# Optimization experiments

Hardware: AMD Instinct MI355X
Metric: run time of the kernel (lower is better)

Reference implementation:

```python
import jax, jax.numpy as jnp
import numpy as np

N_RULE, N_TOKEN = 256, 32000
F_IN, F_ACT, H = 512, 512, 1024  # input_feature_size, action_feature_size, output_feature_size
L, B = 128, 64


def setup_inputs() -> dict:
    key = jax.random.key(0)
    ks = jax.random.split(key, 8)
    s_ih = 1.0 / np.sqrt(H)
    return {
        "input_feature": jax.random.normal(ks[0], (B, F_IN), dtype=jnp.float32),
        "previous_actions": jax.random.randint(ks[1], (L, B, 3), 0, N_RULE, dtype=jnp.int64),
        "mask": jnp.ones((L, B), dtype=jnp.float32),
        "hidden_state": jnp.zeros((B, H), dtype=jnp.float32),
        "state": jnp.zeros((B, H), dtype=jnp.float32),
        "rule_embed": jax.random.normal(ks[2], (N_RULE, F_ACT), dtype=jnp.float32),
        "token_embed": jax.random.normal(ks[3], (N_TOKEN, F_ACT), dtype=jnp.float32),
        "W_ih": jax.random.uniform(ks[4], (4 * H, F_IN + F_ACT), jnp.float32, -s_ih, s_ih),
        "W_hh": jax.random.uniform(ks[5], (4 * H, H), jnp.float32, -s_ih, s_ih),
        "b_ih": jax.random.uniform(ks[6], (4 * H,), jnp.float32, -s_ih, s_ih),
        "b_hh": jax.random.uniform(ks[7], (4 * H,), jnp.float32, -s_ih, s_ih),
    }


def _masked_embed(table, idx):
    # EmbeddingWithMask: index == -1 maps to the zero vector
    valid = (idx != -1)
    emb = table[jnp.where(valid, idx, 0)]
    return emb * valid[..., None].astype(table.dtype)


def reference(input_feature, previous_actions, mask, hidden_state, state,
              rule_embed, token_embed, W_ih, W_hh, b_ih, b_hh):
    prev_rules = previous_actions[..., 0]   # (L, B)
    prev_tokens = previous_actions[..., 1]  # (L, B)
    act = _masked_embed(rule_embed, prev_rules) + _masked_embed(token_embed, prev_tokens)  # (L,B,F_ACT)

    # Per-step input is concat([input_feature, act_t]); precompute the whole
    # input projection x @ W_ih^T + biases once (big batched GEMM).
    l, b = act.shape[0], act.shape[1]
    Wx, Wa = W_ih[:, :input_feature.shape[1]], W_ih[:, input_feature.shape[1]:]
    xg = (input_feature @ Wx.T)[None] + jnp.einsum('lba,ga->lbg', act, Wa) + (b_ih + b_hh)  # (L,B,4H)

    def step(carry, xg_t):
        h, c = carry
        g = xg_t + h @ W_hh.T                     # (B, 4H)
        i, f, gg, o = jnp.split(g, 4, axis=-1)    # torch LSTMCell gate order
        i, f, o = jax.nn.sigmoid(i), jax.nn.sigmoid(f), jax.nn.sigmoid(o)
        c1 = f * c + i * jnp.tanh(gg)
        h1 = o * jnp.tanh(c1)
        return (h1, c1), h1

    (h_n, c_n), hs = jax.lax.scan(step, (hidden_state, state), xg)
    return hs, h_n, c_n
```

## Files before the change

### kernel.cpp

```cpp
#include <hip/hip_runtime.h>
#include <hip/hip_bf16.h>

typedef __attribute__((ext_vector_type(8))) short bf16x8;
typedef __attribute__((ext_vector_type(4))) float f32x4;

#define L_SEQ 128
#define BATCH 64
#define HID   1024
#define GATES 4096
#define NWG   256
#define UPW   4
#define FSTR  32

__device__ inline short f2bf_s(float f) {
  __hip_bfloat16 h = __float2bfloat16(f);
  union { __hip_bfloat16 hh; short s; } u; u.hh = h; return u.s;
}
__device__ inline float sigm(float x) { return 1.f / (1.f + __expf(-x)); }
__device__ inline float tanh_f(float x) {
  x = fminf(x, 15.f);
  float e = __expf(2.f * x);
  return (e - 1.f) / (e + 1.f);
}

__global__ void k_init(const float* __restrict__ hidden, const float* __restrict__ x,
                       const float* __restrict__ bih, const float* __restrict__ bhh,
                       __hip_bfloat16* __restrict__ h_all0, __hip_bfloat16* __restrict__ x_bf,
                       float* __restrict__ bias2, unsigned* __restrict__ bar) {
  int gid = blockIdx.x * 256 + threadIdx.x;
  if (gid < BATCH * HID) h_all0[gid] = __float2bfloat16(hidden[gid]);
  if (gid < BATCH * 512) x_bf[gid]  = __float2bfloat16(x[gid]);
  if (gid < GATES)       bias2[gid] = bih[gid] + bhh[gid];
  if (gid < 16384)       bar[gid] = 0u;
}

__global__ void k_wsplit(const float* __restrict__ Wih,
                         __hip_bfloat16* __restrict__ Wx, __hip_bfloat16* __restrict__ Wa) {
  int e = blockIdx.x * 256 + threadIdx.x;
  int g = e >> 7;
  int ko = (e & 127) << 3;
  const float* src = Wih + (size_t)g * 1024 + ko;
  float4 f0 = *(const float4*)(src);
  float4 f1 = *(const float4*)(src + 4);
  union { bf16x8 v; short s[8]; } o;
  o.s[0]=f2bf_s(f0.x); o.s[1]=f2bf_s(f0.y); o.s[2]=f2bf_s(f0.z); o.s[3]=f2bf_s(f0.w);
  o.s[4]=f2bf_s(f1.x); o.s[5]=f2bf_s(f1.y); o.s[6]=f2bf_s(f1.z); o.s[7]=f2bf_s(f1.w);
  if (ko < 512) *(bf16x8*)(Wx + (size_t)g * 512 + ko)        = o.v;
  else          *(bf16x8*)(Wa + (size_t)g * 512 + (ko - 512)) = o.v;
}

__global__ void k_act(const int* __restrict__ pa, const float* __restrict__ remb,
                      const float* __restrict__ temb, __hip_bfloat16* __restrict__ act) {
  int row = blockIdx.x;
  int tid = threadIdx.x;
  int r  = pa[row * 3 + 0];
  int tk = pa[row * 3 + 1];
  float sr = (r  != -1) ? 1.f : 0.f; int ri = (r  != -1) ? r  : 0;
  float st = (tk != -1) ? 1.f : 0.f; int ti = (tk != -1) ? tk : 0;
  const float4* rr = (const float4*)(remb + (size_t)ri * 512);
  const float4* tr = (const float4*)(temb + (size_t)ti * 512);
  float4 a = rr[tid * 2], b4 = rr[tid * 2 + 1];
  float4 c4 = tr[tid * 2], d4 = tr[tid * 2 + 1];
  union { bf16x8 v; short s[8]; } o;
  o.s[0]=f2bf_s(sr*a.x + st*c4.x);  o.s[1]=f2bf_s(sr*a.y + st*c4.y);
  o.s[2]=f2bf_s(sr*a.z + st*c4.z);  o.s[3]=f2bf_s(sr*a.w + st*c4.w);
  o.s[4]=f2bf_s(sr*b4.x + st*d4.x); o.s[5]=f2bf_s(sr*b4.y + st*d4.y);
  o.s[6]=f2bf_s(sr*b4.z + st*d4.z); o.s[7]=f2bf_s(sr*b4.w + st*d4.w);
  *(bf16x8*)(act + (size_t)row * 512 + tid * 8) = o.v;
}

template<int MODE>
__global__ __launch_bounds__(256) void k_gemm(
    const __hip_bfloat16* __restrict__ A, const __hip_bfloat16* __restrict__ B,
    const float* __restrict__ addend, float* __restrict__ Cf,
    __hip_bfloat16* __restrict__ Cb, int M) {
  __shared__ __hip_bfloat16 At[128][72];
  __shared__ __hip_bfloat16 Bt[128][72];
  const int tid = threadIdx.x;
  const int m0 = blockIdx.y * 128, n0 = blockIdx.x * 128;
  const int w = tid >> 6, lane = tid & 63;
  const int wm = (w >> 1) * 64, wn = (w & 1) * 64;
  const int lm = lane & 15, quad = lane >> 4;
  const int srow = tid >> 1, shalf = (tid & 1) * 32;
  f32x4 acc[4][4] = {};
  for (int k0 = 0; k0 < 512; k0 += 64) {
    int arow = m0 + srow;
    if (MODE == 0 && arow >= M) arow = M - 1;
    const bf16x8* ag = (const bf16x8*)(A + (size_t)arow * 512 + k0 + shalf);
    const bf16x8* bg = (const bf16x8*)(B + (size_t)(n0 + srow) * 512 + k0 + shalf);
    bf16x8 av[4], bv[4];
#pragma unroll
    for (int q = 0; q < 4; ++q) { av[q] = ag[q]; bv[q] = bg[q]; }
    __syncthreads();
#pragma unroll
    for (int q = 0; q < 4; ++q) {
      *(bf16x8*)(&At[srow][shalf + q * 8]) = av[q];
      *(bf16x8*)(&Bt[srow][shalf + q * 8]) = bv[q];
    }
    __syncthreads();
#pragma unroll
    for (int ks = 0; ks < 2; ++ks) {
      bf16x8 af[4], bf[4];
#pragma unroll
      for (int i = 0; i < 4; ++i) {
        af[i] = *(const bf16x8*)(&At[wm + i * 16 + lm][ks * 32 + quad * 8]);
        bf[i] = *(const bf16x8*)(&Bt[wn + i * 16 + lm][ks * 32 + quad * 8]);
      }
#pragma unroll
      for (int i = 0; i < 4; ++i)
#pragma unroll
        for (int j = 0; j < 4; ++j)
          acc[i][j] = __builtin_amdgcn_mfma_f32_16x16x32_bf16(af[i], bf[j], acc[i][j], 0, 0, 0);
    }
  }
#pragma unroll
  for (int i = 0; i < 4; ++i) {
    int mrow = m0 + wm + i * 16 + quad * 4;
#pragma unroll
    for (int j = 0; j < 4; ++j) {
      int ncol = n0 + wn + j * 16 + lm;
#pragma unroll
      for (int r = 0; r < 4; ++r) {
        int m = mrow + r;
        if (MODE == 0) {
          if (m < M) Cf[(size_t)m * GATES + ncol] = acc[i][j][r] + addend[ncol];
        } else {
          float v = acc[i][j][r] + addend[(size_t)(m & 63) * GATES + ncol];
          Cb[(size_t)m * GATES + ncol] = __float2bfloat16(v);
        }
      }
    }
  }
}

__global__ __launch_bounds__(256, 1) void k_scan(
    const float* __restrict__ Whh, const __hip_bfloat16* __restrict__ xg,
    const float* __restrict__ state_in, __hip_bfloat16* __restrict__ h_all,
    float* __restrict__ out_hs, float* __restrict__ out_hn, float* __restrict__ out_cn,
    unsigned* __restrict__ bar) {
  __shared__ __hip_bfloat16 Wl[16 * 1032];
  __shared__ float gl[64 * 17];
  __shared__ unsigned long long hpack[BATCH];
  __shared__ unsigned sdep;
  const int tid = threadIdx.x;
  const int wg = blockIdx.x;
  const int u0 = wg * UPW;
  for (int e = tid; e < 16 * 128; e += 256) {
    int j = e >> 7;
    int ko = (e & 127) << 3;
    int gate = j >> 2, uu = j & 3;
    const float* src = Whh + (size_t)(gate * HID + u0 + uu) * HID + ko;
    float4 f0 = *(const float4*)(src);
    float4 f1 = *(const float4*)(src + 4);
    union { bf16x8 v; short s[8]; } o;
    o.s[0]=f2bf_s(f0.x); o.s[1]=f2bf_s(f0.y); o.s[2]=f2bf_s(f0.z); o.s[3]=f2bf_s(f0.w);
    o.s[4]=f2bf_s(f1.x); o.s[5]=f2bf_s(f1.y); o.s[6]=f2bf_s(f1.z); o.s[7]=f2bf_s(f1.w);
    *(bf16x8*)(&Wl[j * 1032 + ko]) = o.v;
  }
  const int b = tid >> 2, u = tid & 3;
  float c = state_in[b * HID + u0 + u];
  const int w = tid >> 6, lane = tid & 63;
  const int lm = lane & 15, quad = lane >> 4;
  const int m0 = w * 16;
  unsigned* flags = bar;
  unsigned* gen = bar + NWG * FSTR;
  if (tid == 0) sdep = 0;
  const __hip_bfloat16* xgp0 = xg + (size_t)b * GATES + u0 + u;
  float xi  = __bfloat162float(xgp0[0]);
  float xf  = __bfloat162float(xgp0[1024]);
  float xgg = __bfloat162float(xgp0[2048]);
  float xo  = __bfloat162float(xgp0[3072]);
  unsigned dep = 0;
  __syncthreads();
  for (int t = 0; t < L_SEQ; ++t) {
    const __hip_bfloat16* hsrc = h_all + ((size_t)t + dep) * (BATCH * HID);
    const bf16x8* arow = (const bf16x8*)(hsrc + (m0 + lm) * HID + quad * 8);
    bf16x8 areg[32];
#pragma unroll
    for (int kq = 0; kq < 32; ++kq) areg[kq] = arow[kq * 4];
    __builtin_amdgcn_sched_barrier(0);
    f32x4 acc = {0.f, 0.f, 0.f, 0.f};
#pragma unroll
    for (int kq = 0; kq < 32; ++kq) {
      bf16x8 bfrag = *(const bf16x8*)(&Wl[lm * 1032 + kq * 32 + quad * 8]);
      acc = __builtin_amdgcn_mfma_f32_16x16x32_bf16(areg[kq], bfrag, acc, 0, 0, 0);
    }
#pragma unroll
    for (int r = 0; r < 4; ++r) gl[(m0 + quad * 4 + r) * 17 + lm] = acc[r];
    __syncthreads();
    float gi = gl[b * 17 + u]      + xi;
    float gf = gl[b * 17 + 4 + u]  + xf;
    float gg = gl[b * 17 + 8 + u]  + xgg;
    float go = gl[b * 17 + 12 + u] + xo;
    float iv = sigm(gi), fv = sigm(gf), ov = sigm(go), gv = tanh_f(gg);
    c = fv * c + iv * gv;
    float h = ov * tanh_f(c);
    __builtin_nontemporal_store(h, &out_hs[((size_t)t * BATCH + b) * HID + u0 + u]);
    ((unsigned short*)hpack)[b * 4 + u] = (unsigned short)f2bf_s(h);
    if (t == L_SEQ - 1) {
      __builtin_nontemporal_store(h, &out_hn[(size_t)b * HID + u0 + u]);
      __builtin_nontemporal_store(c, &out_cn[(size_t)b * HID + u0 + u]);
    } else {
      const __hip_bfloat16* xgp = xg + ((size_t)(t + 1) * BATCH + b) * GATES + u0 + u;
      float nxi  = __bfloat162float(xgp[0]);
      float nxf  = __bfloat162float(xgp[1024]);
      float nxgg = __bfloat162float(xgp[2048]);
      float nxo  = __bfloat162float(xgp[3072]);
      __syncthreads();
      unsigned long long* hdst64 =
          (unsigned long long*)(h_all + ((size_t)(t + 1)) * (BATCH * HID));
      if (tid < BATCH) {
        __hip_atomic_store(&hdst64[(tid * HID + u0) >> 2], hpack[tid],
                           __ATOMIC_RELAXED, __HIP_MEMORY_SCOPE_SYSTEM);
      }
      unsigned target = (unsigned)(t + 1);
      __builtin_amdgcn_s_waitcnt(0);
      if (wg == 0) {
        if (tid > 0 && tid < NWG) {
          while (__hip_atomic_load(&flags[tid * FSTR], __ATOMIC_RELAXED,
                                   __HIP_MEMORY_SCOPE_SYSTEM) < target)
            __builtin_amdgcn_s_sleep(1);
        }
        __syncthreads();
        if (tid < 32) {
          __hip_atomic_store(&gen[tid * FSTR], target, __ATOMIC_RELAXED,
                             __HIP_MEMORY_SCOPE_SYSTEM);
        }
        dep = 0;
      } else {
        if (tid == 0) {
          __hip_atomic_store(&flags[wg * FSTR], target, __ATOMIC_RELAXED,
                             __HIP_MEMORY_SCOPE_SYSTEM);
          unsigned g;
          do {
            g = __hip_atomic_load(&gen[(wg & 31) * FSTR], __ATOMIC_RELAXED,
                                  __HIP_MEMORY_SCOPE_SYSTEM);
            if (g < target) __builtin_amdgcn_s_sleep(1);
          } while (g < target);
          sdep = g >> 20;
        }
        __syncthreads();
        dep = sdep;
      }
      xi = nxi; xf = nxf; xgg = nxgg; xo = nxo;
    }
  }
}

extern "C" void kernel_launch(void* const* d_in, const int* in_sizes, int n_in,
                              void* d_out, int out_size, void* d_ws, size_t ws_size,
                              hipStream_t stream) {
  const float* x      = (const float*)d_in[0];
  const int*   pa     = (const int*)d_in[1];
  const float* hidden = (const float*)d_in[3];
  const float* state  = (const float*)d_in[4];
  const float* remb   = (const float*)d_in[5];
  const float* temb   = (const float*)d_in[6];
  const float* Wih    = (const float*)d_in[7];
  const float* Whh    = (const float*)d_in[8];
  const float* bih    = (const float*)d_in[9];
  const float* bhh    = (const float*)d_in[10];

  char* ws = (char*)d_ws;
  size_t off = 0;
  auto take = [&](size_t bytes) { char* p = ws + off; off += (bytes + 255) & ~(size_t)255; return p; };
  unsigned* bar         = (unsigned*)take(16384 * 4);
  __hip_bfloat16* h_all = (__hip_bfloat16*)take((size_t)L_SEQ * BATCH * HID * 2);
  __hip_bfloat16* x_bf  = (__hip_bfloat16*)take((size_t)BATCH * 512 * 2);
  float* bias2          = (float*)take((size_t)GATES * 4);
  __hip_bfloat16* Wx    = (__hip_bfloat16*)take((size_t)GATES * 512 * 2);
  __hip_bfloat16* Wa    = (__hip_bfloat16*)take((size_t)GATES * 512 * 2);
  __hip_bfloat16* act   = (__hip_bfloat16*)take((size_t)8192 * 512 * 2);
  float* y0             = (float*)take((size_t)BATCH * GATES * 4);
  __hip_bfloat16* xg    = (__hip_bfloat16*)take((size_t)8192 * GATES * 2);

  float* out_hs = (float*)d_out;
  float* out_hn = out_hs + (size_t)L_SEQ * BATCH * HID;
  float* out_cn = out_hn + (size_t)BATCH * HID;

  hipLaunchKernelGGL(k_init, dim3(256), dim3(256), 0, stream, hidden, x, bih, bhh, h_all, x_bf, bias2, bar);
  hipLaunchKernelGGL(k_wsplit, dim3(2048), dim3(256), 0, stream, Wih, Wx, Wa);
  hipLaunchKernelGGL(k_act, dim3(8192), dim3(64), 0, stream, pa, remb, temb, act);
  hipLaunchKernelGGL((k_gemm<0>), dim3(32, 1), dim3(256), 0, stream,
                     x_bf, Wx, bias2, y0, (__hip_bfloat16*)nullptr, 64);
  hipLaunchKernelGGL((k_gemm<1>), dim3(32, 64), dim3(256), 0, stream,
                     act, Wa, y0, (float*)nullptr, xg, 8192);
  void* args[] = { (void*)&Whh, (void*)&xg, (void*)&state, (void*)&h_all,
                   (void*)&out_hs, (void*)&out_hn, (void*)&out_cn, (void*)&bar };
  (void)hipLaunchCooperativeKernel((void*)k_scan, dim3(NWG), dim3(256), args, 0, stream);
}
```

Baseline: 1.134 ms.

## Use 64 workgroups with 16 units each and decentralized flag barrier

Reduces the persistent LSTM scan from 256 to 64 workgroups, each owning 16 hidden units (64 gate columns) and issuing 4 MFMAs per K step against a larger LDS-resident W_hh slice. The two-level master/generation barrier is replaced by one where every workgroup polls all 64 flags with a wavefront ballot. This drops the extra hop through workgroup 0. Each thread now handles 4 units with vectorized xg loads, h stores and output stores, and the hs store and next xg load are moved after the flag publish to overlap with the wait. The trade is 4x more MFMA work and LDS traffic per workgroup, a larger LDS footprint, and 64 pollers per flag.

```diff
diff --git a/kernel.cpp b/kernel.cpp
--- a/kernel.cpp
+++ b/kernel.cpp
@@ -8,13 +8,16 @@
 #define BATCH 64
 #define HID   1024
 #define GATES 4096
-#define NWG   256
-#define UPW   4
-#define FSTR  32
+#define NWG   64
+#define UPW   16
+#define FSTR  16
 
 __device__ inline short f2bf_s(float f) {
   __hip_bfloat16 h = __float2bfloat16(f);
   union { __hip_bfloat16 hh; short s; } u; u.hh = h; return u.s;
+}
+__device__ inline float bf2f_u(unsigned short s) {
+  union { unsigned u; float f; } u; u.u = ((unsigned)s) << 16; return u.f;
 }
 __device__ inline float sigm(float x) { return 1.f / (1.f + __expf(-x)); }
 __device__ inline float tanh_f(float x) {
@@ -138,17 +141,16 @@
     const float* __restrict__ state_in, __hip_bfloat16* __restrict__ h_all,
     float* __restrict__ out_hs, float* __restrict__ out_hn, float* __restrict__ out_cn,
     unsigned* __restrict__ bar) {
-  __shared__ __hip_bfloat16 Wl[16 * 1032];
-  __shared__ float gl[64 * 17];
-  __shared__ unsigned long long hpack[BATCH];
+  __shared__ __hip_bfloat16 Wl[64 * 1032];
+  __shared__ float gl[64 * 68];
   __shared__ unsigned sdep;
   const int tid = threadIdx.x;
   const int wg = blockIdx.x;
   const int u0 = wg * UPW;
-  for (int e = tid; e < 16 * 128; e += 256) {
+  for (int e = tid; e < 64 * 128; e += 256) {
     int j = e >> 7;
     int ko = (e & 127) << 3;
-    int gate = j >> 2, uu = j & 3;
+    int gate = j >> 4, uu = j & 15;
     const float* src = Whh + (size_t)(gate * HID + u0 + uu) * HID + ko;
     float4 f0 = *(const float4*)(src);
     float4 f1 = *(const float4*)(src + 4);
@@ -157,19 +159,21 @@
     o.s[4]=f2bf_s(f1.x); o.s[5]=f2bf_s(f1.y); o.s[6]=f2bf_s(f1.z); o.s[7]=f2bf_s(f1.w);
     *(bf16x8*)(&Wl[j * 1032 + ko]) = o.v;
   }
-  const int b = tid >> 2, u = tid & 3;
-  float c = state_in[b * HID + u0 + u];
+  const int b = tid >> 2, x = tid & 3;
+  f32x4 c4i = *(const f32x4*)(state_in + (size_t)b * HID + u0 + x * 4);
+  float cc[4] = {c4i[0], c4i[1], c4i[2], c4i[3]};
   const int w = tid >> 6, lane = tid & 63;
   const int lm = lane & 15, quad = lane >> 4;
   const int m0 = w * 16;
   unsigned* flags = bar;
-  unsigned* gen = bar + NWG * FSTR;
   if (tid == 0) sdep = 0;
-  const __hip_bfloat16* xgp0 = xg + (size_t)b * GATES + u0 + u;
-  float xi  = __bfloat162float(xgp0[0]);
-  float xf  = __bfloat162float(xgp0[1024]);
-  float xgg = __bfloat162float(xgp0[2048]);
-  float xo  = __bfloat162float(xgp0[3072]);
+  union U64 { unsigned long long u; unsigned short s[4]; };
+  U64 xv[4];
+  {
+    const unsigned short* xp = (const unsigned short*)xg + (size_t)b * GATES + u0 + x * 4;
+#pragma unroll
+    for (int g = 0; g < 4; ++g) xv[g].u = *(const unsigned long long*)(xp + g * 1024);
+  }
   unsigned dep = 0;
   __syncthreads();
   for (int t = 0; t < L_SEQ; ++t) {
@@ -179,70 +183,80 @@
 #pragma unroll
     for (int kq = 0; kq < 32; ++kq) areg[kq] = arow[kq * 4];
     __builtin_amdgcn_sched_barrier(0);
-    f32x4 acc = {0.f, 0.f, 0.f, 0.f};
+    f32x4 acc[4] = {{0.f, 0.f, 0.f, 0.f}, {0.f, 0.f, 0.f, 0.f},
+                    {0.f, 0.f, 0.f, 0.f}, {0.f, 0.f, 0.f, 0.f}};
 #pragma unroll
     for (int kq = 0; kq < 32; ++kq) {
-      bf16x8 bfrag = *(const bf16x8*)(&Wl[lm * 1032 + kq * 32 + quad * 8]);
-      acc = __builtin_amdgcn_mfma_f32_16x16x32_bf16(areg[kq], bfrag, acc, 0, 0, 0);
-    }
-#pragma unroll
-    for (int r = 0; r < 4; ++r) gl[(m0 + quad * 4 + r) * 17 + lm] = acc[r];
+#pragma unroll
+      for (int n = 0; n < 4; ++n) {
+        bf16x8 bfrag = *(const bf16x8*)(&Wl[(n * 16 + lm) * 1032 + kq * 32 + quad * 8]);
+        acc[n] = __builtin_amdgcn_mfma_f32_16x16x32_bf16(areg[kq], bfrag, acc[n], 0, 0, 0);
+      }
+    }
+#pragma unroll
+    for (int n = 0; n < 4; ++n)
+#pragma unroll
+      for (int r = 0; r < 4; ++r)
+        gl[(m0 + quad * 4 + r) * 68 + n * 16 + lm] = acc[n][r];
     __syncthreads();
-    float gi = gl[b * 17 + u]      + xi;
-    float gf = gl[b * 17 + 4 + u]  + xf;
-    float gg = gl[b * 17 + 8 + u]  + xgg;
-    float go = gl[b * 17 + 12 + u] + xo;
-    float iv = sigm(gi), fv = sigm(gf), ov = sigm(go), gv = tanh_f(gg);
-    c = fv * c + iv * gv;
-    float h = ov * tanh_f(c);
-    __builtin_nontemporal_store(h, &out_hs[((size_t)t * BATCH + b) * HID + u0 + u]);
-    ((unsigned short*)hpack)[b * 4 + u] = (unsigned short)f2bf_s(h);
+    f32x4 gi4 = *(const f32x4*)(&gl[b * 68 + 0  + x * 4]);
+    f32x4 gf4 = *(const f32x4*)(&gl[b * 68 + 16 + x * 4]);
+    f32x4 gg4 = *(const f32x4*)(&gl[b * 68 + 32 + x * 4]);
+    f32x4 go4 = *(const f32x4*)(&gl[b * 68 + 48 + x * 4]);
+    float hv[4];
+    U64 hp;
+#pragma unroll
+    for (int j = 0; j < 4; ++j) {
+      float ii = sigm(gi4[j] + bf2f_u(xv[0].s[j]));
+      float ff = sigm(gf4[j] + bf2f_u(xv[1].s[j]));
+      float gv = tanh_f(gg4[j] + bf2f_u(xv[2].s[j]));
+      float oo = sigm(go4[j] + bf2f_u(xv[3].s[j]));
+      cc[j] = ff * cc[j] + ii * gv;
+      hv[j] = oo * tanh_f(cc[j]);
+      hp.s[j] = (unsigned short)f2bf_s(hv[j]);
+    }
+    f32x4 hv4 = {hv[0], hv[1], hv[2], hv[3]};
+    float* hsout = out_hs + ((size_t)t * BATCH + b) * HID + u0 + x * 4;
     if (t == L_SEQ - 1) {
-      __builtin_nontemporal_store(h, &out_hn[(size_t)b * HID + u0 + u]);
-      __builtin_nontemporal_store(c, &out_cn[(size_t)b * HID + u0 + u]);
+      __builtin_nontemporal_store(hv4, (f32x4*)hsout);
+      f32x4 cc4 = {cc[0], cc[1], cc[2], cc[3]};
+      __builtin_nontemporal_store(hv4, (f32x4*)(out_hn + (size_t)b * HID + u0 + x * 4));
+      __builtin_nontemporal_store(cc4, (f32x4*)(out_cn + (size_t)b * HID + u0 + x * 4));
     } else {
-      const __hip_bfloat16* xgp = xg + ((size_t)(t + 1) * BATCH + b) * GATES + u0 + u;
-      float nxi  = __bfloat162float(xgp[0]);
-      float nxf  = __bfloat162float(xgp[1024]);
-      float nxgg = __bfloat162float(xgp[2048]);
-      float nxo  = __bfloat162float(xgp[3072]);
-      __syncthreads();
-      unsigned long long* hdst64 =
+      unsigned long long* hdst =
           (unsigned long long*)(h_all + ((size_t)(t + 1)) * (BATCH * HID));
-      if (tid < BATCH) {
-        __hip_atomic_store(&hdst64[(tid * HID + u0) >> 2], hpack[tid],
-                           __ATOMIC_RELAXED, __HIP_MEMORY_SCOPE_SYSTEM);
-      }
+      __hip_atomic_store(&hdst[(((size_t)b * HID + u0) >> 2) + x], hp.u,
+                         __ATOMIC_RELAXED, __HIP_MEMORY_SCOPE_SYSTEM);
       unsigned target = (unsigned)(t + 1);
       __builtin_amdgcn_s_waitcnt(0);
-      if (wg == 0) {
-        if (tid > 0 && tid < NWG) {
-          while (__hip_atomic_load(&flags[tid * FSTR], __ATOMIC_RELAXED,
-                                   __HIP_MEMORY_SCOPE_SYSTEM) < target)
-            __builtin_amdgcn_s_sleep(1);
+      if (tid == 0)
+        __hip_atomic_store(&flags[wg * FSTR], target, __ATOMIC_RELAXED,
+                           __HIP_MEMORY_SCOPE_SYSTEM);
+      __builtin_amdgcn_sched_barrier(0);
+      __builtin_nontemporal_store(hv4, (f32x4*)hsout);
+      {
+        const unsigned short* xp = (const unsigned short*)xg +
+            ((size_t)(t + 1) * BATCH + b) * GATES + u0 + x * 4;
+#pragma unroll
+        for (int g = 0; g < 4; ++g) xv[g].u = *(const unsigned long long*)(xp + g * 1024);
+      }
+      if (tid < NWG) {
+        bool ok = false;
+        unsigned long long bl;
+        for (;;) {
+          if (!ok) {
+            unsigned v = __hip_atomic_load(&flags[tid * FSTR], __ATOMIC_RELAXED,
+                                           __HIP_MEMORY_SCOPE_SYSTEM);
+            ok = (v >= target);
+          }
+          bl = __ballot(ok);
+          if (bl == 0xFFFFFFFFFFFFFFFFull) break;
+          __builtin_amdgcn_s_sleep(1);
         }
-        __syncthreads();
-        if (tid < 32) {
-          __hip_atomic_store(&gen[tid * FSTR], target, __ATOMIC_RELAXED,
-                             __HIP_MEMORY_SCOPE_SYSTEM);
-        }
-        dep = 0;
-      } else {
-        if (tid == 0) {
-          __hip_atomic_store(&flags[wg * FSTR], target, __ATOMIC_RELAXED,
-                             __HIP_MEMORY_SCOPE_SYSTEM);
-          unsigned g;
-          do {
-            g = __hip_atomic_load(&gen[(wg & 31) * FSTR], __ATOMIC_RELAXED,
-                                  __HIP_MEMORY_SCOPE_SYSTEM);
-            if (g < target) __builtin_amdgcn_s_sleep(1);
-          } while (g < target);
-          sdep = g >> 20;
-        }
-        __syncthreads();
-        dep = sdep;
-      }
-      xi = nxi; xf = nxf; xgg = nxgg; xo = nxo;
+        if (tid == 0) sdep = (unsigned)((bl >> 44) >> 20);
+      }
+      __syncthreads();
+      dep = sdep;
     }
   }
 }
```

After: 1.158 ms. 1.02x slower.

## Replace master-gather grid barrier with all-to-all flag polling and relayout W in LDS

Applied to the files above, without the earlier changes.

The two-level grid barrier (workgroup 0 gathers all flags, then broadcasts a generation word) becomes a flat barrier. Every thread of every workgroup polls one workgroup's flag directly, which cuts one round-trip of cross-CU latency per timestep. The out_hs store and the next-step xg loads move after the flag publish so they overlap the barrier wait. The W_hh tile in LDS is relaid out kq-major without padding and the MFMA chain is split into two accumulators to shorten the dependency chain. The price is 256x more polling traffic on the flag lines, and the flag stride is shrunk so flags share cache lines.

```diff
diff --git a/kernel.cpp b/kernel.cpp
--- a/kernel.cpp
+++ b/kernel.cpp
@@ -10,7 +10,7 @@
 #define GATES 4096
 #define NWG   256
 #define UPW   4
-#define FSTR  32
+#define FSTR  4
 
 __device__ inline short f2bf_s(float f) {
   __hip_bfloat16 h = __float2bfloat16(f);
@@ -138,10 +138,9 @@
     const float* __restrict__ state_in, __hip_bfloat16* __restrict__ h_all,
     float* __restrict__ out_hs, float* __restrict__ out_hn, float* __restrict__ out_cn,
     unsigned* __restrict__ bar) {
-  __shared__ __hip_bfloat16 Wl[16 * 1032];
+  __shared__ __hip_bfloat16 Wl[16 * 1024];
   __shared__ float gl[64 * 17];
   __shared__ unsigned long long hpack[BATCH];
-  __shared__ unsigned sdep;
   const int tid = threadIdx.x;
   const int wg = blockIdx.x;
   const int u0 = wg * UPW;
@@ -155,7 +154,8 @@
     union { bf16x8 v; short s[8]; } o;
     o.s[0]=f2bf_s(f0.x); o.s[1]=f2bf_s(f0.y); o.s[2]=f2bf_s(f0.z); o.s[3]=f2bf_s(f0.w);
     o.s[4]=f2bf_s(f1.x); o.s[5]=f2bf_s(f1.y); o.s[6]=f2bf_s(f1.z); o.s[7]=f2bf_s(f1.w);
-    *(bf16x8*)(&Wl[j * 1032 + ko]) = o.v;
+    int kq = ko >> 5, qd = (ko >> 3) & 3;
+    *(bf16x8*)(&Wl[kq * 512 + j * 32 + qd * 8]) = o.v;
   }
   const int b = tid >> 2, u = tid & 3;
   float c = state_in[b * HID + u0 + u];
@@ -163,8 +163,7 @@
   const int lm = lane & 15, quad = lane >> 4;
   const int m0 = w * 16;
   unsigned* flags = bar;
-  unsigned* gen = bar + NWG * FSTR;
-  if (tid == 0) sdep = 0;
+  const __hip_bfloat16* Wb = Wl + lm * 32 + quad * 8;
   const __hip_bfloat16* xgp0 = xg + (size_t)b * GATES + u0 + u;
   float xi  = __bfloat162float(xgp0[0]);
   float xf  = __bfloat162float(xgp0[1024]);
@@ -179,14 +178,17 @@
 #pragma unroll
     for (int kq = 0; kq < 32; ++kq) areg[kq] = arow[kq * 4];
     __builtin_amdgcn_sched_barrier(0);
-    f32x4 acc = {0.f, 0.f, 0.f, 0.f};
-#pragma unroll
-    for (int kq = 0; kq < 32; ++kq) {
-      bf16x8 bfrag = *(const bf16x8*)(&Wl[lm * 1032 + kq * 32 + quad * 8]);
-      acc = __builtin_amdgcn_mfma_f32_16x16x32_bf16(areg[kq], bfrag, acc, 0, 0, 0);
-    }
-#pragma unroll
-    for (int r = 0; r < 4; ++r) gl[(m0 + quad * 4 + r) * 17 + lm] = acc[r];
+    f32x4 acc0 = {0.f, 0.f, 0.f, 0.f}, acc1 = {0.f, 0.f, 0.f, 0.f};
+#pragma unroll
+    for (int kq = 0; kq < 32; kq += 2) {
+      acc0 = __builtin_amdgcn_mfma_f32_16x16x32_bf16(
+          areg[kq], *(const bf16x8*)(Wb + (size_t)kq * 512), acc0, 0, 0, 0);
+      acc1 = __builtin_amdgcn_mfma_f32_16x16x32_bf16(
+          areg[kq + 1], *(const bf16x8*)(Wb + (size_t)(kq + 1) * 512), acc1, 0, 0, 0);
+    }
+    f32x4 accs = acc0 + acc1;
+#pragma unroll
+    for (int r = 0; r < 4; ++r) gl[(m0 + quad * 4 + r) * 17 + lm] = accs[r];
     __syncthreads();
     float gi = gl[b * 17 + u]      + xi;
     float gf = gl[b * 17 + 4 + u]  + xf;
@@ -195,17 +197,12 @@
     float iv = sigm(gi), fv = sigm(gf), ov = sigm(go), gv = tanh_f(gg);
     c = fv * c + iv * gv;
     float h = ov * tanh_f(c);
-    __builtin_nontemporal_store(h, &out_hs[((size_t)t * BATCH + b) * HID + u0 + u]);
-    ((unsigned short*)hpack)[b * 4 + u] = (unsigned short)f2bf_s(h);
     if (t == L_SEQ - 1) {
+      __builtin_nontemporal_store(h, &out_hs[((size_t)t * BATCH + b) * HID + u0 + u]);
       __builtin_nontemporal_store(h, &out_hn[(size_t)b * HID + u0 + u]);
       __builtin_nontemporal_store(c, &out_cn[(size_t)b * HID + u0 + u]);
     } else {
-      const __hip_bfloat16* xgp = xg + ((size_t)(t + 1) * BATCH + b) * GATES + u0 + u;
-      float nxi  = __bfloat162float(xgp[0]);
-      float nxf  = __bfloat162float(xgp[1024]);
-      float nxgg = __bfloat162float(xgp[2048]);
-      float nxo  = __bfloat162float(xgp[3072]);
+      ((unsigned short*)hpack)[b * 4 + u] = (unsigned short)f2bf_s(h);
       __syncthreads();
       unsigned long long* hdst64 =
           (unsigned long long*)(h_all + ((size_t)(t + 1)) * (BATCH * HID));
@@ -215,33 +212,25 @@
       }
       unsigned target = (unsigned)(t + 1);
       __builtin_amdgcn_s_waitcnt(0);
-      if (wg == 0) {
-        if (tid > 0 && tid < NWG) {
-          while (__hip_atomic_load(&flags[tid * FSTR], __ATOMIC_RELAXED,
-                                   __HIP_MEMORY_SCOPE_SYSTEM) < target)
-            __builtin_amdgcn_s_sleep(1);
-        }
-        __syncthreads();
-        if (tid < 32) {
-          __hip_atomic_store(&gen[tid * FSTR], target, __ATOMIC_RELAXED,
-                             __HIP_MEMORY_SCOPE_SYSTEM);
-        }
-        dep = 0;
-      } else {
-        if (tid == 0) {
-          __hip_atomic_store(&flags[wg * FSTR], target, __ATOMIC_RELAXED,
-                             __HIP_MEMORY_SCOPE_SYSTEM);
-          unsigned g;
-          do {
-            g = __hip_atomic_load(&gen[(wg & 31) * FSTR], __ATOMIC_RELAXED,
-                                  __HIP_MEMORY_SCOPE_SYSTEM);
-            if (g < target) __builtin_amdgcn_s_sleep(1);
-          } while (g < target);
-          sdep = g >> 20;
-        }
-        __syncthreads();
-        dep = sdep;
-      }
+      if (tid == 0)
+        __hip_atomic_store(&flags[wg * FSTR], target, __ATOMIC_RELAXED,
+                           __HIP_MEMORY_SCOPE_SYSTEM);
+      __builtin_amdgcn_sched_barrier(0);
+      __builtin_nontemporal_store(h, &out_hs[((size_t)t * BATCH + b) * HID + u0 + u]);
+      const __hip_bfloat16* xgp = xg + ((size_t)(t + 1) * BATCH + b) * GATES + u0 + u;
+      float nxi  = __bfloat162float(xgp[0]);
+      float nxf  = __bfloat162float(xgp[1024]);
+      float nxgg = __bfloat162float(xgp[2048]);
+      float nxo  = __bfloat162float(xgp[3072]);
+      unsigned v;
+      for (;;) {
+        v = __hip_atomic_load(&flags[tid * FSTR], __ATOMIC_RELAXED,
+                              __HIP_MEMORY_SCOPE_SYSTEM);
+        if (v >= target) break;
+        __builtin_amdgcn_s_sleep(1);
+      }
+      dep = v >> 20;
+      __syncthreads();
       xi = nxi; xf = nxf; xgg = nxgg; xo = nxo;
     }
   }
```

Result: no change. 1.146 ms (+1.0%).
